# Performance work log

Measured on AMD Instinct MI355X. Metric: run time of the kernel, lower is better.

The kernel has to match this reference:

```python
import jax, jax.numpy as jnp
import numpy as np

CP = (96, 96, 96)      # control-point grid size (D, H, W)
NSTEPS = 7             # VecInt int_steps
N_TP = 4               # timepoints
# all ordered pairs i<j: tid 'ti_to_tj' -> ref=i, flo=j  (K = 6)
REF_IDX = np.array([0, 0, 0, 1, 1, 2])
FLO_IDX = np.array([1, 2, 3, 2, 3, 3])


def _make_grid(shape):
    axes = [jnp.arange(s, dtype=jnp.float32) for s in shape]
    return jnp.stack(jnp.meshgrid(*axes, indexing='ij'), axis=0)  # (3, D, H, W)

GRID = _make_grid(CP)


def trilinear_sample(vol, coords):
    """Sample channels-first volume at absolute voxel coordinates.

    vol:    (C, D, H, W) field values
    coords: (3, D, H, W) absolute (i, j, k) voxel coordinates
    returns (C, D, H, W); border (clamp) handling at edges.
    """
    D, H, W = vol.shape[1:]
    x, y, z = coords[0], coords[1], coords[2]
    x0f = jnp.floor(x); y0f = jnp.floor(y); z0f = jnp.floor(z)
    fx = x - x0f; fy = y - y0f; fz = z - z0f
    x0 = jnp.clip(x0f.astype(jnp.int32), 0, D - 1)
    x1 = jnp.clip(x0 + 1, 0, D - 1)
    y0 = jnp.clip(y0f.astype(jnp.int32), 0, H - 1)
    y1 = jnp.clip(y0 + 1, 0, H - 1)
    z0 = jnp.clip(z0f.astype(jnp.int32), 0, W - 1)
    z1 = jnp.clip(z0 + 1, 0, W - 1)

    c000 = vol[:, x0, y0, z0]; c001 = vol[:, x0, y0, z1]
    c010 = vol[:, x0, y1, z0]; c011 = vol[:, x0, y1, z1]
    c100 = vol[:, x1, y0, z0]; c101 = vol[:, x1, y0, z1]
    c110 = vol[:, x1, y1, z0]; c111 = vol[:, x1, y1, z1]

    c00 = c000 * (1 - fz) + c001 * fz
    c01 = c010 * (1 - fz) + c011 * fz
    c10 = c100 * (1 - fz) + c101 * fz
    c11 = c110 * (1 - fz) + c111 * fz
    c0 = c00 * (1 - fy) + c01 * fy
    c1 = c10 * (1 - fy) + c11 * fy
    return c0 * (1 - fx) + c1 * fx


def vecint(v):
    """Scaling-and-squaring integration of stationary velocity field v: (3,D,H,W)."""
    v = v * (1.0 / 2.0 ** NSTEPS)
    for _ in range(NSTEPS):
        v = v + trilinear_sample(v, GRID + v)
    return v


def compose_fields(f1, f2):
    """(grid + f1 + f2(grid + f1)) - grid, fields (3,D,H,W)."""
    return f1 + trilinear_sample(f2, GRID + f1)


def setup_inputs() -> dict:
    key = jax.random.key(0)
    k1, k2 = jax.random.split(key)
    T = jax.random.normal(k1, (N_TP, 3) + CP, dtype=jnp.float32)
    R = jax.random.normal(k2, CP + (3, len(REF_IDX)), dtype=jnp.float32)
    return {"T": T, "R": R}


def reference(T, R):
    # integrate +/- velocity for every timepoint once (same math as per-pair calls)
    F_pos = jax.vmap(vecint)(T)           # (N, 3, D, H, W) = integrate(T[t])
    F_neg = jax.vmap(vecint)(-T)          # (N, 3, D, H, W) = integrate(-T[t])
    ref = jnp.asarray(REF_IDX)
    flo = jnp.asarray(FLO_IDX)
    # R_hat[k] = compose(integrate(-T[ref_k]), integrate(T[flo_k]))  -> (K,3,D,H,W)
    R_hat = jax.vmap(compose_fields)(F_neg[ref], F_pos[flo])
    # original permutes R_hat to (D,H,W,3,K); equivalently permute R the other way
    residue = R_hat - jnp.transpose(R, (4, 3, 0, 1, 2))  # (K,3,D,H,W)
    # l1 cost: sum_k,x sqrt(sum_c residue^2)
    loss = jnp.sum(jnp.sqrt(jnp.sum(residue ** 2, axis=1)))
    return loss
```

## Files before the change

kernel.cpp:

```cpp
#include <hip/hip_runtime.h>
#include <hip/hip_fp16.h>

#define NV    884736
#define NB    3456
#define DIM   96
#define DIM2  9216


union H4 { uint2 u; __half2 h2[2]; };
union H8 { uint4 u; __half2 h2[4]; };

struct F3 { float x, y, z; };

__device__ __forceinline__ F3 lerp3(F3 a, F3 b, float t, float omt) {
    F3 r;
    r.x = a.x * omt + b.x * t;
    r.y = a.y * omt + b.y * t;
    r.z = a.z * omt + b.z * t;
    return r;
}

__device__ __forceinline__ uint2 pack_h4(float x, float y, float z) {
    H4 v;
    v.h2[0] = __floats2half2_rn(x, y);
    v.h2[1] = __floats2half2_rn(z, 0.0f);
    return v.u;
}

__device__ __forceinline__ F3 unpack_h4(uint2 raw) {
    H4 v; v.u = raw;
    float2 xy = __half22float2(v.h2[0]);
    float2 zp = __half22float2(v.h2[1]);
    F3 r; r.x = xy.x; r.y = xy.y; r.z = zp.x;
    return r;
}

struct TriIdx { int idx[4]; float fx, fy, fz; };

__device__ __forceinline__ TriIdx tri_prep(float x, float y, float z) {
    TriIdx t;
    float xf = floorf(x), yf = floorf(y), zf = floorf(z);
    t.fx = x - xf; t.fy = y - yf;
    float fz = z - zf;
    int x0 = (int)xf; x0 = x0 < 0 ? 0 : (x0 > DIM - 1 ? DIM - 1 : x0);
    int y0 = (int)yf; y0 = y0 < 0 ? 0 : (y0 > DIM - 1 ? DIM - 1 : y0);
    int z0 = (int)zf; z0 = z0 < 0 ? 0 : (z0 > DIM - 1 ? DIM - 1 : z0);
    int x1 = x0 + 1; if (x1 > DIM - 1) x1 = DIM - 1;
    int y1 = y0 + 1; if (y1 > DIM - 1) y1 = DIM - 1;
    t.fz = (z0 < DIM - 1) ? fz : 0.0f;
    int X0 = x0 * DIM2, X1 = x1 * DIM2;
    int Y0 = y0 * DIM,  Y1 = y1 * DIM;
    t.idx[0] = X0 + Y0 + z0;
    t.idx[1] = X0 + Y1 + z0;
    t.idx[2] = X1 + Y0 + z0;
    t.idx[3] = X1 + Y1 + z0;
    return t;
}

__device__ __forceinline__ void tri_gather(const uint2* __restrict__ f,
                                           const TriIdx& t, H8 c[4]) {
    #pragma unroll
    for (int q = 0; q < 4; q++)
        c[q].u = *(const uint4*)(f + t.idx[q]);
}

__device__ __forceinline__ F3 tri_combine(const TriIdx& t, const H8 c[4]) {
    float gz = 1.0f - t.fz, gy = 1.0f - t.fy, gx = 1.0f - t.fx;
    F3 pz[4];
    #pragma unroll
    for (int q = 0; q < 4; q++) {
        float2 xy0 = __half22float2(c[q].h2[0]);
        float2 z0p = __half22float2(c[q].h2[1]);
        float2 xy1 = __half22float2(c[q].h2[2]);
        float2 z1p = __half22float2(c[q].h2[3]);
        F3 lo; lo.x = xy0.x; lo.y = xy0.y; lo.z = z0p.x;
        F3 hi; hi.x = xy1.x; hi.y = xy1.y; hi.z = z1p.x;
        pz[q] = lerp3(lo, hi, t.fz, gz);
    }
    F3 c0 = lerp3(pz[0], pz[1], t.fy, gy);
    F3 c1 = lerp3(pz[2], pz[3], t.fy, gy);
    return lerp3(c0, c1, t.fx, gx);
}

__global__ __launch_bounds__(256) void init_kernel(const float* __restrict__ T,
                                                   uint2* __restrict__ bufA,
                                                   float* __restrict__ out) {
    int t = blockIdx.y;
    int l = blockIdx.x * 256 + threadIdx.x;
    if (t == 0 && l == 0) out[0] = 0.0f;
    const float inv = 1.0f / 128.0f;
    float vx = T[(size_t)(t * 3 + 0) * NV + l] * inv;
    float vy = T[(size_t)(t * 3 + 1) * NV + l] * inv;
    float vz = T[(size_t)(t * 3 + 2) * NV + l] * inv;
    bufA[(size_t)t * NV + l]       = pack_h4( vx,  vy,  vz);
    bufA[(size_t)(t + 4) * NV + l] = pack_h4(-vx, -vy, -vz);
}

__global__ __launch_bounds__(256) void step_kernel(const uint2* __restrict__ src,
                                                   uint2* __restrict__ dst) {
    int g  = blockIdx.x;
    int f  = g & 7;
    int vb = g >> 3;
    const uint2* __restrict__ s = src + (size_t)f * NV;
    uint2*       __restrict__ d = dst + (size_t)f * NV;

    int l   = vb * 256 + threadIdx.x;
    int i   = l / DIM2;
    int rem = l % DIM2;
    int j   = rem / DIM;
    int k   = rem % DIM;

    F3 v = unpack_h4(s[l]);
    TriIdx t = tri_prep((float)i + v.x, (float)j + v.y, (float)k + v.z);
    H8 c[4];
    tri_gather(s, t, c);
    F3 smp = tri_combine(t, c);
    d[l] = pack_h4(v.x + smp.x, v.y + smp.y, v.z + smp.z);
}

__global__ __launch_bounds__(256) void loss_kernel(const uint2* __restrict__ fields,
                                                   const float* __restrict__ R,
                                                   float* __restrict__ out) {
    int l = blockIdx.x * 256 + threadIdx.x;
    int k = l % DIM;
    int j = (l / DIM) % DIM;
    int i = l / DIM2;
    float fi = (float)i, fj = (float)j, fk = (float)k;

    F3 f1c[3];
    #pragma unroll
    for (int r = 0; r < 3; r++)
        f1c[r] = unpack_h4(fields[(size_t)(4 + r) * NV + l]);

    float rbuf[18];
    const float* Rl = R + (size_t)l * 18;
    #pragma unroll
    for (int q = 0; q < 18; q++) rbuf[q] = Rl[q];

    const int REFI[6] = {0, 0, 0, 1, 1, 2};
    const int FLOI[6] = {1, 2, 3, 2, 3, 3};

    float acc = 0.0f;
    #pragma unroll
    for (int p = 0; p < 6; p += 2) {
        F3 f1a = f1c[REFI[p]];
        F3 f1b = f1c[REFI[p + 1]];
        const uint2* __restrict__ f2a = fields + (size_t)FLOI[p]     * NV;
        const uint2* __restrict__ f2b = fields + (size_t)FLOI[p + 1] * NV;
        TriIdx ta = tri_prep(fi + f1a.x, fj + f1a.y, fk + f1a.z);
        TriIdx tb = tri_prep(fi + f1b.x, fj + f1b.y, fk + f1b.z);
        H8 ca[4], cb[4];
        tri_gather(f2a, ta, ca);
        tri_gather(f2b, tb, cb);
        F3 sa = tri_combine(ta, ca);
        F3 sb = tri_combine(tb, cb);
        float rx = f1a.x + sa.x - rbuf[0 * 6 + p];
        float ry = f1a.y + sa.y - rbuf[1 * 6 + p];
        float rz = f1a.z + sa.z - rbuf[2 * 6 + p];
        acc += sqrtf(rx * rx + ry * ry + rz * rz);
        rx = f1b.x + sb.x - rbuf[0 * 6 + p + 1];
        ry = f1b.y + sb.y - rbuf[1 * 6 + p + 1];
        rz = f1b.z + sb.z - rbuf[2 * 6 + p + 1];
        acc += sqrtf(rx * rx + ry * ry + rz * rz);
    }

    __shared__ float wsum[4];
    int lane = threadIdx.x & 63;
    int wid  = threadIdx.x >> 6;
    #pragma unroll
    for (int off = 32; off > 0; off >>= 1)
        acc += __shfl_down(acc, off, 64);
    if (lane == 0) wsum[wid] = acc;
    __syncthreads();
    if (threadIdx.x == 0) {
        float s = wsum[0] + wsum[1] + wsum[2] + wsum[3];
        atomicAdd(out, s);
    }
}

extern "C" void kernel_launch(void* const* d_in, const int* in_sizes, int n_in,
                              void* d_out, int out_size, void* d_ws, size_t ws_size,
                              hipStream_t stream) {
    const float* T = (const float*)d_in[0];
    const float* R = (const float*)d_in[1];
    float* out = (float*)d_out;

    uint2* bufA = (uint2*)d_ws;
    uint2* bufB = bufA + (size_t)8 * NV + 32;

    dim3 blk(256);
    init_kernel<<<dim3(NB, 4), blk, 0, stream>>>(T, bufA, out);

    uint2* src = bufA;
    uint2* dst = bufB;
    for (int s = 0; s < 7; s++) {
        step_kernel<<<NB * 8, blk, 0, stream>>>(src, dst);
        uint2* tmp = src; src = dst; dst = tmp;
    }
    loss_kernel<<<NB, blk, 0, stream>>>(src, R, out);
}
```

Measured before the change: 398.0 us.

## Integrate only the six needed fields and process four voxels per thread

The loss only uses positive fields for timepoints 1-3 and negative fields for 0-2, so the unused ones are no longer integrated. This cuts the scaling-and-squaring work from 8 fields to 6. The step kernel now handles 4 consecutive voxels per thread with vectorized loads and stores, to get more gathers in flight. The loss kernel issues its gathers earlier to overlap memory latency, at the cost of higher register pressure; the slack region past the buffers is zeroed for the over-reading gathers.

```diff
diff --git a/kernel.cpp b/kernel.cpp
--- a/kernel.cpp
+++ b/kernel.cpp
@@ -5,6 +5,9 @@
 #define NB    3456
 #define DIM   96
 #define DIM2  9216
+#define NF    6
+#define VPT   4
+#define SLACK 32
 
 
 union H4 { uint2 u; __half2 h2[2]; };
@@ -84,83 +87,119 @@
 
 __global__ __launch_bounds__(256) void init_kernel(const float* __restrict__ T,
                                                    uint2* __restrict__ bufA,
+                                                   uint2* __restrict__ bufB,
                                                    float* __restrict__ out) {
     int t = blockIdx.y;
     int l = blockIdx.x * 256 + threadIdx.x;
     if (t == 0 && l == 0) out[0] = 0.0f;
+    if (t == 0 && l < SLACK) {
+        bufA[(size_t)NF * NV + l] = make_uint2(0u, 0u);
+        bufB[(size_t)NF * NV + l] = make_uint2(0u, 0u);
+    }
     const float inv = 1.0f / 128.0f;
     float vx = T[(size_t)(t * 3 + 0) * NV + l] * inv;
     float vy = T[(size_t)(t * 3 + 1) * NV + l] * inv;
     float vz = T[(size_t)(t * 3 + 2) * NV + l] * inv;
-    bufA[(size_t)t * NV + l]       = pack_h4( vx,  vy,  vz);
-    bufA[(size_t)(t + 4) * NV + l] = pack_h4(-vx, -vy, -vz);
-}
-
-__global__ __launch_bounds__(256) void step_kernel(const uint2* __restrict__ src,
-                                                   uint2* __restrict__ dst) {
+    if (t >= 1) bufA[(size_t)(t - 1) * NV + l] = pack_h4( vx,  vy,  vz);
+    if (t <= 2) bufA[(size_t)(t + 3) * NV + l] = pack_h4(-vx, -vy, -vz);
+}
+
+__global__ __launch_bounds__(256, 4) void step_kernel(const uint2* __restrict__ src,
+                                                      uint2* __restrict__ dst) {
     int g  = blockIdx.x;
-    int f  = g & 7;
-    int vb = g >> 3;
+    int f  = g % NF;
+    int vb = g / NF;
     const uint2* __restrict__ s = src + (size_t)f * NV;
     uint2*       __restrict__ d = dst + (size_t)f * NV;
 
-    int l   = vb * 256 + threadIdx.x;
-    int i   = l / DIM2;
-    int rem = l % DIM2;
+    int l0  = (vb * 256 + (int)threadIdx.x) * VPT;
+    int i   = l0 / DIM2;
+    int rem = l0 - i * DIM2;
     int j   = rem / DIM;
-    int k   = rem % DIM;
-
-    F3 v = unpack_h4(s[l]);
-    TriIdx t = tri_prep((float)i + v.x, (float)j + v.y, (float)k + v.z);
-    H8 c[4];
-    tri_gather(s, t, c);
-    F3 smp = tri_combine(t, c);
-    d[l] = pack_h4(v.x + smp.x, v.y + smp.y, v.z + smp.z);
-}
-
-__global__ __launch_bounds__(256) void loss_kernel(const uint2* __restrict__ fields,
-                                                   const float* __restrict__ R,
-                                                   float* __restrict__ out) {
+    int k0  = rem - j * DIM;
+    float fi = (float)i, fj = (float)j;
+
+    uint4 o01 = *(const uint4*)(s + l0);
+    uint4 o23 = *(const uint4*)(s + l0 + 2);
+    F3 v[VPT];
+    v[0] = unpack_h4(make_uint2(o01.x, o01.y));
+    v[1] = unpack_h4(make_uint2(o01.z, o01.w));
+    v[2] = unpack_h4(make_uint2(o23.x, o23.y));
+    v[3] = unpack_h4(make_uint2(o23.z, o23.w));
+
+    TriIdx t[VPT];
+    #pragma unroll
+    for (int m = 0; m < VPT; m++)
+        t[m] = tri_prep(fi + v[m].x, fj + v[m].y, (float)(k0 + m) + v[m].z);
+
+    H8 c[VPT][4];
+    #pragma unroll
+    for (int m = 0; m < VPT; m++)
+        tri_gather(s, t[m], c[m]);
+
+    uint4 w01, w23;
+    {
+        F3 r0 = tri_combine(t[0], c[0]);
+        F3 r1 = tri_combine(t[1], c[1]);
+        uint2 p0 = pack_h4(v[0].x + r0.x, v[0].y + r0.y, v[0].z + r0.z);
+        uint2 p1 = pack_h4(v[1].x + r1.x, v[1].y + r1.y, v[1].z + r1.z);
+        w01.x = p0.x; w01.y = p0.y; w01.z = p1.x; w01.w = p1.y;
+    }
+    {
+        F3 r2 = tri_combine(t[2], c[2]);
+        F3 r3 = tri_combine(t[3], c[3]);
+        uint2 p2 = pack_h4(v[2].x + r2.x, v[2].y + r2.y, v[2].z + r2.z);
+        uint2 p3 = pack_h4(v[3].x + r3.x, v[3].y + r3.y, v[3].z + r3.z);
+        w23.x = p2.x; w23.y = p2.y; w23.z = p3.x; w23.w = p3.y;
+    }
+    *(uint4*)(d + l0)     = w01;
+    *(uint4*)(d + l0 + 2) = w23;
+}
+
+__global__ __launch_bounds__(256, 4) void loss_kernel(const uint2* __restrict__ fields,
+                                                      const float* __restrict__ R,
+                                                      float* __restrict__ out) {
     int l = blockIdx.x * 256 + threadIdx.x;
     int k = l % DIM;
     int j = (l / DIM) % DIM;
     int i = l / DIM2;
     float fi = (float)i, fj = (float)j, fk = (float)k;
 
-    F3 f1c[3];
-    #pragma unroll
-    for (int r = 0; r < 3; r++)
-        f1c[r] = unpack_h4(fields[(size_t)(4 + r) * NV + l]);
-
     float rbuf[18];
     const float* Rl = R + (size_t)l * 18;
     #pragma unroll
     for (int q = 0; q < 18; q++) rbuf[q] = Rl[q];
 
+    F3 f1c[3];
+    #pragma unroll
+    for (int r = 0; r < 3; r++)
+        f1c[r] = unpack_h4(fields[(size_t)(3 + r) * NV + l]);
+
     const int REFI[6] = {0, 0, 0, 1, 1, 2};
-    const int FLOI[6] = {1, 2, 3, 2, 3, 3};
+    const int FLOF[6] = {0, 1, 2, 1, 2, 2};
+
+    TriIdx t[6];
+    #pragma unroll
+    for (int p = 0; p < 6; p++) {
+        F3 f1 = f1c[REFI[p]];
+        t[p] = tri_prep(fi + f1.x, fj + f1.y, fk + f1.z);
+    }
+
+    H8 c[6][4];
+    #pragma unroll
+    for (int p = 0; p < 3; p++)
+        tri_gather(fields + (size_t)FLOF[p] * NV, t[p], c[p]);
 
     float acc = 0.0f;
     #pragma unroll
-    for (int p = 0; p < 6; p += 2) {
-        F3 f1a = f1c[REFI[p]];
-        F3 f1b = f1c[REFI[p + 1]];
-        const uint2* __restrict__ f2a = fields + (size_t)FLOI[p]     * NV;
-        const uint2* __restrict__ f2b = fields + (size_t)FLOI[p + 1] * NV;
-        TriIdx ta = tri_prep(fi + f1a.x, fj + f1a.y, fk + f1a.z);
-        TriIdx tb = tri_prep(fi + f1b.x, fj + f1b.y, fk + f1b.z);
-        H8 ca[4], cb[4];
-        tri_gather(f2a, ta, ca);
-        tri_gather(f2b, tb, cb);
-        F3 sa = tri_combine(ta, ca);
-        F3 sb = tri_combine(tb, cb);
-        float rx = f1a.x + sa.x - rbuf[0 * 6 + p];
-        float ry = f1a.y + sa.y - rbuf[1 * 6 + p];
-        float rz = f1a.z + sa.z - rbuf[2 * 6 + p];
-        acc += sqrtf(rx * rx + ry * ry + rz * rz);
-        rx = f1b.x + sb.x - rbuf[0 * 6 + p + 1];
-        ry = f1b.y + sb.y - rbuf[1 * 6 + p + 1];
-        rz = f1b.z + sb.z - rbuf[2 * 6 + p + 1];
+    for (int p = 0; p < 6; p++) {
+        F3 smp = tri_combine(t[p], c[p]);
+        if (p + 3 < 6)
+            tri_gather(fields + (size_t)FLOF[p + 3] * NV, t[p + 3], c[p + 3]);
+        F3 f1 = f1c[REFI[p]];
+        float rx = f1.x + smp.x - rbuf[0 * 6 + p];
+        float ry = f1.y + smp.y - rbuf[1 * 6 + p];
+        float rz = f1.z + smp.z - rbuf[2 * 6 + p];
         acc += sqrtf(rx * rx + ry * ry + rz * rz);
     }
 
@@ -186,15 +225,16 @@
     float* out = (float*)d_out;
 
     uint2* bufA = (uint2*)d_ws;
-    uint2* bufB = bufA + (size_t)8 * NV + 32;
+    uint2* bufB = bufA + (size_t)NF * NV + SLACK;
 
     dim3 blk(256);
-    init_kernel<<<dim3(NB, 4), blk, 0, stream>>>(T, bufA, out);
+    init_kernel<<<dim3(NB, 4), blk, 0, stream>>>(T, bufA, bufB, out);
 
     uint2* src = bufA;
     uint2* dst = bufB;
+    const int step_blocks = (NV / (256 * VPT)) * NF;
     for (int s = 0; s < 7; s++) {
-        step_kernel<<<NB * 8, blk, 0, stream>>>(src, dst);
+        step_kernel<<<step_blocks, blk, 0, stream>>>(src, dst);
         uint2* tmp = src; src = dst; dst = tmp;
     }
     loss_kernel<<<NB, blk, 0, stream>>>(src, R, out);
```

Measured after the change: 502.6 us. 26.3% more time.

## Integrate only six needed fields, two voxels per thread, chunked block mapping

Applied to the files above, without the earlier changes.

The step kernel now integrates only the six fields the loss actually uses (positive T1..T3, negative T0..T2) and drops the two unused ones, since pos T0 and neg T3 never appear in any pair. Each thread now handles two consecutive voxels with vectorized 16-byte load and store. Blocks are remapped so that consecutive block IDs interleave across chunks, which is meant to improve cache locality across field boundaries. A zeroed slack region is added after the fields so over-reads past the end stay defined, and the loss kernel's field indices are remapped to the new layout.

```diff
diff --git a/kernel.cpp b/kernel.cpp
--- a/kernel.cpp
+++ b/kernel.cpp
@@ -5,6 +5,9 @@
 #define NB    3456
 #define DIM   96
 #define DIM2  9216
+#define NF    6
+#define VPT   2
+#define SLACK 32
 
 
 union H4 { uint2 u; __half2 h2[2]; };
@@ -84,38 +87,63 @@
 
 __global__ __launch_bounds__(256) void init_kernel(const float* __restrict__ T,
                                                    uint2* __restrict__ bufA,
+                                                   uint2* __restrict__ bufB,
                                                    float* __restrict__ out) {
     int t = blockIdx.y;
     int l = blockIdx.x * 256 + threadIdx.x;
     if (t == 0 && l == 0) out[0] = 0.0f;
+    if (t == 0 && l < SLACK) {
+        bufA[(size_t)NF * NV + l] = make_uint2(0u, 0u);
+        bufB[(size_t)NF * NV + l] = make_uint2(0u, 0u);
+    }
     const float inv = 1.0f / 128.0f;
     float vx = T[(size_t)(t * 3 + 0) * NV + l] * inv;
     float vy = T[(size_t)(t * 3 + 1) * NV + l] * inv;
     float vz = T[(size_t)(t * 3 + 2) * NV + l] * inv;
-    bufA[(size_t)t * NV + l]       = pack_h4( vx,  vy,  vz);
-    bufA[(size_t)(t + 4) * NV + l] = pack_h4(-vx, -vy, -vz);
-}
-
+    if (t >= 1) bufA[(size_t)(t - 1) * NV + l] = pack_h4( vx,  vy,  vz);
+    if (t <= 2) bufA[(size_t)(t + 3) * NV + l] = pack_h4(-vx, -vy, -vz);
+}
+
+#define STEP_VB   (NV / (256 * VPT))
+#define STEP_W    (STEP_VB * NF)
+#define STEP_CHK  (STEP_W / 8)
 __global__ __launch_bounds__(256) void step_kernel(const uint2* __restrict__ src,
                                                    uint2* __restrict__ dst) {
-    int g  = blockIdx.x;
-    int f  = g & 7;
-    int vb = g >> 3;
+    int b   = blockIdx.x;
+    int w   = (b & 7) * STEP_CHK + (b >> 3);
+    int f   = w / STEP_VB;
+    int vb  = w - f * STEP_VB;
     const uint2* __restrict__ s = src + (size_t)f * NV;
     uint2*       __restrict__ d = dst + (size_t)f * NV;
 
-    int l   = vb * 256 + threadIdx.x;
-    int i   = l / DIM2;
-    int rem = l % DIM2;
+    int l0  = (vb * 256 + (int)threadIdx.x) * VPT;
+    int i   = l0 / DIM2;
+    int rem = l0 - i * DIM2;
     int j   = rem / DIM;
-    int k   = rem % DIM;
-
-    F3 v = unpack_h4(s[l]);
-    TriIdx t = tri_prep((float)i + v.x, (float)j + v.y, (float)k + v.z);
-    H8 c[4];
-    tri_gather(s, t, c);
-    F3 smp = tri_combine(t, c);
-    d[l] = pack_h4(v.x + smp.x, v.y + smp.y, v.z + smp.z);
+    int k0  = rem - j * DIM;
+    float fi = (float)i, fj = (float)j;
+
+    uint4 o01 = *(const uint4*)(s + l0);
+    F3 v[VPT];
+    v[0] = unpack_h4(make_uint2(o01.x, o01.y));
+    v[1] = unpack_h4(make_uint2(o01.z, o01.w));
+
+    TriIdx t[VPT];
+    #pragma unroll
+    for (int m = 0; m < VPT; m++)
+        t[m] = tri_prep(fi + v[m].x, fj + v[m].y, (float)(k0 + m) + v[m].z);
+
+    H8 c[VPT][4];
+    #pragma unroll
+    for (int m = 0; m < VPT; m++)
+        tri_gather(s, t[m], c[m]);
+
+    F3 r0 = tri_combine(t[0], c[0]);
+    F3 r1 = tri_combine(t[1], c[1]);
+    uint2 p0 = pack_h4(v[0].x + r0.x, v[0].y + r0.y, v[0].z + r0.z);
+    uint2 p1 = pack_h4(v[1].x + r1.x, v[1].y + r1.y, v[1].z + r1.z);
+    uint4 wv; wv.x = p0.x; wv.y = p0.y; wv.z = p1.x; wv.w = p1.y;
+    *(uint4*)(d + l0) = wv;
 }
 
 __global__ __launch_bounds__(256) void loss_kernel(const uint2* __restrict__ fields,
@@ -130,7 +158,7 @@
     F3 f1c[3];
     #pragma unroll
     for (int r = 0; r < 3; r++)
-        f1c[r] = unpack_h4(fields[(size_t)(4 + r) * NV + l]);
+        f1c[r] = unpack_h4(fields[(size_t)(3 + r) * NV + l]);
 
     float rbuf[18];
     const float* Rl = R + (size_t)l * 18;
@@ -138,15 +166,15 @@
     for (int q = 0; q < 18; q++) rbuf[q] = Rl[q];
 
     const int REFI[6] = {0, 0, 0, 1, 1, 2};
-    const int FLOI[6] = {1, 2, 3, 2, 3, 3};
+    const int FLOF[6] = {0, 1, 2, 1, 2, 2};
 
     float acc = 0.0f;
     #pragma unroll
     for (int p = 0; p < 6; p += 2) {
         F3 f1a = f1c[REFI[p]];
         F3 f1b = f1c[REFI[p + 1]];
-        const uint2* __restrict__ f2a = fields + (size_t)FLOI[p]     * NV;
-        const uint2* __restrict__ f2b = fields + (size_t)FLOI[p + 1] * NV;
+        const uint2* __restrict__ f2a = fields + (size_t)FLOF[p]     * NV;
+        const uint2* __restrict__ f2b = fields + (size_t)FLOF[p + 1] * NV;
         TriIdx ta = tri_prep(fi + f1a.x, fj + f1a.y, fk + f1a.z);
         TriIdx tb = tri_prep(fi + f1b.x, fj + f1b.y, fk + f1b.z);
         H8 ca[4], cb[4];
@@ -186,15 +214,15 @@
     float* out = (float*)d_out;
 
     uint2* bufA = (uint2*)d_ws;
-    uint2* bufB = bufA + (size_t)8 * NV + 32;
+    uint2* bufB = bufA + (size_t)NF * NV + SLACK;
 
     dim3 blk(256);
-    init_kernel<<<dim3(NB, 4), blk, 0, stream>>>(T, bufA, out);
+    init_kernel<<<dim3(NB, 4), blk, 0, stream>>>(T, bufA, bufB, out);
 
     uint2* src = bufA;
     uint2* dst = bufB;
     for (int s = 0; s < 7; s++) {
-        step_kernel<<<NB * 8, blk, 0, stream>>>(src, dst);
+        step_kernel<<<STEP_W, blk, 0, stream>>>(src, dst);
         uint2* tmp = src; src = dst; dst = tmp;
     }
     loss_kernel<<<NB, blk, 0, stream>>>(src, R, out);
```

Result: faster. 350.2 us (-12.0%).
